# Kernel tuning notes

Hardware: AMD Instinct MI355X
Metric: run time of the kernel (lower is better)

Reference implementation:

```python
import jax, jax.numpy as jnp
import numpy as np

EPS = 1e-6
GROUPS = 32


def setup_inputs() -> dict:
    key = jax.random.key(0)
    ks = jax.random.split(key, 6)
    B, C, T = 4, 256, 4096
    s = 1.0 / np.sqrt(C)
    return {
        "x": jax.random.normal(ks[0], (B, C, T), dtype=jnp.float32),
        "gn_scale": jnp.ones((C,), jnp.float32),
        "gn_bias": jnp.zeros((C,), jnp.float32),
        "wq": jax.random.normal(ks[1], (C, C), jnp.float32) * s,
        "bq": jnp.zeros((C,), jnp.float32),
        "wk": jax.random.normal(ks[2], (C, C), jnp.float32) * s,
        "bk": jnp.zeros((C,), jnp.float32),
        "wv": jax.random.normal(ks[3], (C, C), jnp.float32) * s,
        "bv": jnp.zeros((C,), jnp.float32),
        "wo": jax.random.normal(ks[4], (C, C), jnp.float32) * s,
        "bo": jnp.zeros((C,), jnp.float32),
    }


def _group_norm(x, scale, bias):
    B, C, T = x.shape
    h = x.reshape(B, GROUPS, C // GROUPS, T)
    mean = h.mean(axis=(2, 3), keepdims=True)
    var = ((h - mean) ** 2).mean(axis=(2, 3), keepdims=True)
    h = (h - mean) * jax.lax.rsqrt(var + EPS)
    h = h.reshape(B, C, T)
    return h * scale[None, :, None] + bias[None, :, None]


def _conv1x1(w, b, h):
    # Conv1d kernel_size=1 == per-timestep channel matmul
    return jnp.einsum('oc,bct->bot', w, h) + b[None, :, None]


def reference(x, gn_scale, gn_bias, wq, bq, wk, bk, wv, bv, wo, bo):
    B, C, T = x.shape
    h = _group_norm(x, gn_scale, gn_bias)
    q = _conv1x1(wq, bq, h)  # [B,C,T]
    k = _conv1x1(wk, bk, h)
    v = _conv1x1(wv, bv, h)
    # w_[b,q,k] = sum_c q[b,c,q] k[b,c,k] * C**-0.5, softmax over k
    w = jnp.einsum('bcq,bck->bqk', q, k) * (C ** -0.5)
    w = jax.nn.softmax(w, axis=2)
    # torch code: h_[b, i, c] = sum_j w[b, j, i] * v_perm[b, j, c]
    h = jnp.einsum('bqk,bcq->bck', w, v)  # [B,C,T]
    h = _conv1x1(wo, bo, h)
    return x + h
```

## Files before the change

kernel.cpp:

```cpp
#include <hip/hip_runtime.h>

typedef float f32x4 __attribute__((ext_vector_type(4)));
typedef short s16x8 __attribute__((ext_vector_type(8)));

#define MOFF 12.0f

__device__ __forceinline__ unsigned short f2bf(float f) {
  unsigned int u = __float_as_uint(f);
  u += 0x7fffu + ((u >> 16) & 1u);
  return (unsigned short)(u >> 16);
}

template <typename T>
__device__ __forceinline__ void gload16(const T* g, T* l) {
  __builtin_amdgcn_global_load_lds(
      (const __attribute__((address_space(1))) void*)g,
      (__attribute__((address_space(3))) void*)l, 16, 0, 0);
}

__global__ __launch_bounds__(256) void gn_stats_k(const float* __restrict__ x,
                                                  float* __restrict__ meanv,
                                                  float* __restrict__ rstdv) {
  const int bg = blockIdx.x;
  const float4* base = (const float4*)(x + (size_t)bg * 8 * 4096);
  float s = 0.f, q = 0.f;
  for (int i = threadIdx.x; i < 8192; i += 256) {
    float4 v = base[i];
    s += v.x + v.y + v.z + v.w;
    q += v.x * v.x + v.y * v.y + v.z * v.z + v.w * v.w;
  }
  for (int o = 32; o; o >>= 1) { s += __shfl_down(s, o); q += __shfl_down(q, o); }
  __shared__ float ss[4], sq[4];
  const int wv = threadIdx.x >> 6;
  if ((threadIdx.x & 63) == 0) { ss[wv] = s; sq[wv] = q; }
  __syncthreads();
  if (threadIdx.x == 0) {
    s = ss[0] + ss[1] + ss[2] + ss[3];
    q = sq[0] + sq[1] + sq[2] + sq[3];
    float mu = s * (1.f / 32768.f);
    float var = q * (1.f / 32768.f) - mu * mu;
    meanv[bg] = mu;
    rstdv[bg] = rsqrtf(var + 1e-6f);
  }
}

__global__ __launch_bounds__(256) void gn_apply_t_k(const float* __restrict__ x,
    const float* __restrict__ gamma, const float* __restrict__ beta,
    const float* __restrict__ meanv, const float* __restrict__ rstdv,
    unsigned short* __restrict__ hT) {
  __shared__ unsigned short tile[64][72];
  const int b = blockIdx.z, c0 = blockIdx.y * 64, t0 = blockIdx.x * 64;
  const int tid = threadIdx.x;
  {
    const int tr = tid >> 4, tc = (tid & 15) * 4;
    const float* xb = x + ((size_t)b * 256 + c0) * 4096 + t0;
    for (int p2 = 0; p2 < 4; ++p2) {
      int cl = p2 * 16 + tr;
      int c = c0 + cl;
      int bg = b * 32 + (c >> 3);
      float ga = gamma[c] * rstdv[bg];
      float be = beta[c] - meanv[bg] * ga;
      float4 v = *(const float4*)(xb + (size_t)cl * 4096 + tc);
      tile[cl][tc + 0] = f2bf(v.x * ga + be);
      tile[cl][tc + 1] = f2bf(v.y * ga + be);
      tile[cl][tc + 2] = f2bf(v.z * ga + be);
      tile[cl][tc + 3] = f2bf(v.w * ga + be);
    }
  }
  __syncthreads();
  {
    const int orow = tid >> 3, oc = (tid & 7) * 8;
    unsigned short* hb = hT + ((size_t)b * 4096 + t0) * 256 + c0;
    for (int p2 = 0; p2 < 2; ++p2) {
      int tl = p2 * 32 + orow;
      s16x8 w;
#pragma unroll
      for (int j = 0; j < 8; ++j) w[j] = (short)tile[oc + j][tl];
      *(s16x8*)(hb + (size_t)tl * 256 + oc) = w;
    }
  }
}

enum { EPI_WT = 0, EPI_PB = 1, EPI_FIN = 3, EPI_PBR = 4 };

template <bool AF32, int EPI>
__global__ __launch_bounds__(256) void gemm64_k(
    const void* __restrict__ Ap, long long sA, int lda,
    const unsigned short* __restrict__ Bp, long long sB, int ldb,
    void* __restrict__ Op, long long sO, int ldo,
    const float* __restrict__ bias,
    const float* __restrict__ xadd, long long sX,
    float scale, int K) {
  __shared__ s16x8 lsA[4][64];
  __shared__ s16x8 lsB[4][64];
  const int tid = threadIdx.x;
  const int m0 = blockIdx.y * 64, n0 = blockIdx.x * 64;
  const int z = blockIdx.z;
  const int lane = tid & 63, wv = tid >> 6;
  const int lrow = lane & 15, lg = lane >> 4;
  const int srow = tid >> 2, scg = tid & 3;
  const int swrow = srow ^ (scg << 1);

  f32x4 acc[4];
#pragma unroll
  for (int i = 0; i < 4; ++i) acc[i] = (f32x4){0.f, 0.f, 0.f, 0.f};

  const unsigned short* Bb = Bp + (size_t)z * sB + (size_t)(n0 + srow) * ldb + scg * 8;

  for (int k0 = 0; k0 < K; k0 += 32) {
    if (AF32) {
      const float* ap = (const float*)Ap + (size_t)z * sA + (size_t)(m0 + srow) * lda + k0 + scg * 8;
      float4 v0 = *(const float4*)ap;
      float4 v1 = *(const float4*)(ap + 4);
      s16x8 w;
      w[0] = (short)f2bf(v0.x); w[1] = (short)f2bf(v0.y);
      w[2] = (short)f2bf(v0.z); w[3] = (short)f2bf(v0.w);
      w[4] = (short)f2bf(v1.x); w[5] = (short)f2bf(v1.y);
      w[6] = (short)f2bf(v1.z); w[7] = (short)f2bf(v1.w);
      lsA[scg][swrow] = w;
    } else {
      const unsigned short* ap = (const unsigned short*)Ap + (size_t)z * sA + (size_t)(m0 + srow) * lda + k0 + scg * 8;
      lsA[scg][swrow] = *(const s16x8*)ap;
    }
    lsB[scg][swrow] = *(const s16x8*)(Bb + k0);
    __syncthreads();
    s16x8 af = lsA[lg][(wv * 16 + lrow) ^ (lg << 1)];
#pragma unroll
    for (int nt = 0; nt < 4; ++nt) {
      s16x8 bf = lsB[lg][(nt * 16 + lrow) ^ (lg << 1)];
      acc[nt] = __builtin_amdgcn_mfma_f32_16x16x32_bf16(af, bf, acc[nt], 0, 0, 0);
    }
    __syncthreads();
  }

  const int mb = m0 + wv * 16 + lg * 4;
  float bv0 = 0.f, bv1 = 0.f, bv2 = 0.f, bv3 = 0.f;
  if (bias) { bv0 = bias[mb]; bv1 = bias[mb + 1]; bv2 = bias[mb + 2]; bv3 = bias[mb + 3]; }
#pragma unroll
  for (int nt = 0; nt < 4; ++nt) {
    const int n = n0 + nt * 16 + lrow;
    if (EPI == EPI_WT) {
      ushort4 pk;
      pk.x = f2bf((acc[nt][0] + bv0) * scale);
      pk.y = f2bf((acc[nt][1] + bv1) * scale);
      pk.z = f2bf((acc[nt][2] + bv2) * scale);
      pk.w = f2bf((acc[nt][3] + bv3) * scale);
      *(ushort4*)((unsigned short*)Op + (size_t)z * sO + (size_t)n * ldo + mb) = pk;
    } else if (EPI == EPI_PB) {
      unsigned short* o = (unsigned short*)Op + (size_t)z * sO;
      o[(size_t)(mb + 0) * ldo + n] = f2bf(acc[nt][0] + bv0);
      o[(size_t)(mb + 1) * ldo + n] = f2bf(acc[nt][1] + bv1);
      o[(size_t)(mb + 2) * ldo + n] = f2bf(acc[nt][2] + bv2);
      o[(size_t)(mb + 3) * ldo + n] = f2bf(acc[nt][3] + bv3);
    } else if (EPI == EPI_PBR) {
      unsigned short* o = (unsigned short*)Op + (size_t)z * sO;
      const float rc = (xadd + (size_t)z * sX)[n];
      o[(size_t)(mb + 0) * ldo + n] = f2bf((acc[nt][0] + bv0) * rc);
      o[(size_t)(mb + 1) * ldo + n] = f2bf((acc[nt][1] + bv1) * rc);
      o[(size_t)(mb + 2) * ldo + n] = f2bf((acc[nt][2] + bv2) * rc);
      o[(size_t)(mb + 3) * ldo + n] = f2bf((acc[nt][3] + bv3) * rc);
    } else {
      float* o = (float*)Op + (size_t)z * sO;
      const float* xa = xadd + (size_t)z * sX;
      o[(size_t)(mb + 0) * ldo + n] = acc[nt][0] + bv0 + xa[(size_t)(mb + 0) * ldo + n];
      o[(size_t)(mb + 1) * ldo + n] = acc[nt][1] + bv1 + xa[(size_t)(mb + 1) * ldo + n];
      o[(size_t)(mb + 2) * ldo + n] = acc[nt][2] + bv2 + xa[(size_t)(mb + 2) * ldo + n];
      o[(size_t)(mb + 3) * ldo + n] = acc[nt][3] + bv3 + xa[(size_t)(mb + 3) * ldo + n];
    }
  }
}

__global__ __launch_bounds__(256) void attn_stats3_k(
    const unsigned short* __restrict__ qT,
    const unsigned short* __restrict__ kT,
    float* __restrict__ pl) {
  __shared__ unsigned short kbuf[2][64 * 256];
  const int tid = threadIdx.x;
  const int b = blockIdx.z;
  const int Q0 = blockIdx.x * 256;
  const int kc = blockIdx.y;
  const int lane = tid & 63, wq = tid >> 6;
  const int lrow = lane & 15, lg = lane >> 4;

  const unsigned short* qb = qT + (size_t)b * (4096 * 256);
  const unsigned short* kb = kT + (size_t)b * (4096 * 256);

  s16x8 af[4][8];
#pragma unroll
  for (int mt = 0; mt < 4; ++mt)
#pragma unroll
    for (int ks = 0; ks < 8; ++ks)
      af[mt][ks] = *(const s16x8*)(qb + (size_t)(Q0 + wq * 64 + mt * 16 + lrow) * 256 + ks * 32 + lg * 8);

  float sl[4][4];
#pragma unroll
  for (int mt = 0; mt < 4; ++mt)
#pragma unroll
    for (int j = 0; j < 4; ++j) sl[mt][j] = 0.f;

  int cur = 0;
  {
    const unsigned short* src = kb + (size_t)(kc * 512) * 256;
#pragma unroll
    for (int rep = 0; rep < 8; ++rep) {
      int i = rep * 256 + tid;
      int row = i >> 5, c8 = i & 31;
      gload16(src + (size_t)row * 256 + (c8 ^ (row & 7)) * 8, &kbuf[0][(i - lane) * 8]);
    }
  }
  __syncthreads();

  for (int it = 0; it < 8; ++it) {
    if (it + 1 < 8) {
      const unsigned short* src = kb + (size_t)(kc * 512 + (it + 1) * 64) * 256;
#pragma unroll
      for (int rep = 0; rep < 8; ++rep) {
        int i = rep * 256 + tid;
        int row = i >> 5, c8 = i & 31;
        gload16(src + (size_t)row * 256 + (c8 ^ (row & 7)) * 8, &kbuf[cur ^ 1][(i - lane) * 8]);
      }
    }
#pragma unroll
    for (int nt = 0; nt < 4; ++nt) {
      f32x4 acc[4];
#pragma unroll
      for (int mt = 0; mt < 4; ++mt) acc[mt] = (f32x4){0.f, 0.f, 0.f, 0.f};
#pragma unroll
      for (int ks = 0; ks < 8; ++ks) {
        int row = nt * 16 + lrow;
        int ch = (ks * 4 + lg) ^ (row & 7);
        s16x8 bf = *(const s16x8*)&kbuf[cur][row * 256 + ch * 8];
#pragma unroll
        for (int mt = 0; mt < 4; ++mt)
          acc[mt] = __builtin_amdgcn_mfma_f32_16x16x32_bf16(af[mt][ks], bf, acc[mt], 0, 0, 0);
      }
#pragma unroll
      for (int mt = 0; mt < 4; ++mt)
#pragma unroll
        for (int j = 0; j < 4; ++j) sl[mt][j] += __expf(acc[mt][j] - MOFF);
    }
    __syncthreads();
    cur ^= 1;
  }
#pragma unroll
  for (int mt = 0; mt < 4; ++mt)
#pragma unroll
    for (int j = 0; j < 4; ++j) {
      float v = sl[mt][j];
      v += __shfl_xor(v, 1);
      v += __shfl_xor(v, 2);
      v += __shfl_xor(v, 4);
      v += __shfl_xor(v, 8);
      sl[mt][j] = v;
    }
  if (lrow == 0) {
    float* plb = pl + ((size_t)kc * 4 + b) * 4096;
#pragma unroll
    for (int mt = 0; mt < 4; ++mt)
#pragma unroll
      for (int j = 0; j < 4; ++j)
        plb[Q0 + wq * 64 + mt * 16 + lg * 4 + j] = sl[mt][j];
  }
}

__global__ __launch_bounds__(256) void make_r_k(const float* __restrict__ pl,
                                                float* __restrict__ ra) {
  int i = blockIdx.x * 256 + threadIdx.x;
  int b = i >> 12, q = i & 4095;
  float l = 0.f;
#pragma unroll
  for (int kc = 0; kc < 8; ++kc) l += pl[((size_t)kc * 4 + b) * 4096 + q];
  ra[i] = 1.f / l;
}

__global__ __launch_bounds__(512) void attn_pv6e_k(
    const unsigned short* __restrict__ qT,
    const unsigned short* __restrict__ kT,
    const unsigned short* __restrict__ vt,
    unsigned short* __restrict__ aT) {
  __shared__ unsigned short qbuf[2][64 * 256];
  __shared__ unsigned short P[64 * 64];
  const int tid = threadIdx.x;
  const int pidx = blockIdx.x;
  const int z = (pidx >> 1) & 3;
  const int kt = ((pidx >> 3) << 1) | (pidx & 1);
  const int K0 = kt * 64;
  const int lane = tid & 63, w = tid >> 6;
  const int lrow = lane & 15, lg = lane >> 4;
  const int khw = w >> 2;
  const int qqw = w & 3;

  const unsigned short* qg = qT + (size_t)z * (4096 * 256);
  const unsigned short* kg = kT + (size_t)z * (4096 * 256);
  const unsigned short* vg = vt + (size_t)z * (4096 * 256);

  s16x8 kf[2][8];
#pragma unroll
  for (int ktl = 0; ktl < 2; ++ktl)
#pragma unroll
    for (int ks = 0; ks < 8; ++ks)
      kf[ktl][ks] = *(const s16x8*)(kg + (size_t)(K0 + khw * 32 + ktl * 16 + lrow) * 256 + ks * 32 + lg * 8);

  f32x4 oacc[2][4];
#pragma unroll
  for (int ct = 0; ct < 2; ++ct)
#pragma unroll
    for (int nt = 0; nt < 4; ++nt) oacc[ct][nt] = (f32x4){0.f, 0.f, 0.f, 0.f};

  int cur = 0;
  {
#pragma unroll
    for (int rep = 0; rep < 4; ++rep) {
      int i = rep * 512 + tid;
      int row = i >> 5, c8 = i & 31;
      gload16(qg + (size_t)row * 256 + (c8 ^ (row & 7)) * 8, &qbuf[0][(i - lane) * 8]);
    }
  }
  __syncthreads();

  for (int qi = 0; qi < 64; ++qi) {
    const int q0 = qi * 64;
    s16x8 vf[2][2];
#pragma unroll
    for (int ct = 0; ct < 2; ++ct)
#pragma unroll
      for (int qs = 0; qs < 2; ++qs)
        vf[ct][qs] = *(const s16x8*)(vg + (size_t)(w * 32 + ct * 16 + lrow) * 4096 + q0 + qs * 32 + lg * 8);
    if (qi + 1 < 64) {
      const unsigned short* src = qg + (size_t)(q0 + 64) * 256;
#pragma unroll
      for (int rep = 0; rep < 4; ++rep) {
        int i = rep * 512 + tid;
        int row = i >> 5, c8 = i & 31;
        gload16(src + (size_t)row * 256 + (c8 ^ (row & 7)) * 8, &qbuf[cur ^ 1][(i - lane) * 8]);
      }
    }
    f32x4 sacc[2];
    sacc[0] = (f32x4){0.f, 0.f, 0.f, 0.f};
    sacc[1] = (f32x4){0.f, 0.f, 0.f, 0.f};
#pragma unroll
    for (int ks = 0; ks < 8; ++ks) {
      int row = qqw * 16 + lrow;
      int ch = (ks * 4 + lg) ^ (row & 7);
      s16x8 qf = *(const s16x8*)&qbuf[cur][row * 256 + ch * 8];
      sacc[0] = __builtin_amdgcn_mfma_f32_16x16x32_bf16(kf[0][ks], qf, sacc[0], 0, 0, 0);
      sacc[1] = __builtin_amdgcn_mfma_f32_16x16x32_bf16(kf[1][ks], qf, sacc[1], 0, 0, 0);
    }
    {
      const int ql = qqw * 16 + lrow;
#pragma unroll
      for (int ktl = 0; ktl < 2; ++ktl)
#pragma unroll
        for (int j = 0; j < 4; ++j) {
          int k = khw * 32 + ktl * 16 + lg * 4 + j;
          float p = __expf(sacc[ktl][j] - MOFF);
          P[k * 64 + (((ql >> 3) ^ (k & 7)) << 3) + (ql & 7)] = f2bf(p);
        }
    }
    __syncthreads();
#pragma unroll
    for (int qs = 0; qs < 2; ++qs) {
      s16x8 pf[4];
#pragma unroll
      for (int nt = 0; nt < 4; ++nt) {
        int k = nt * 16 + lrow;
        pf[nt] = *(const s16x8*)&P[k * 64 + (((qs * 4 + lg) ^ (k & 7)) << 3)];
      }
#pragma unroll
      for (int ct = 0; ct < 2; ++ct)
#pragma unroll
        for (int nt = 0; nt < 4; ++nt)
          oacc[ct][nt] = __builtin_amdgcn_mfma_f32_16x16x32_bf16(vf[ct][qs], pf[nt], oacc[ct][nt], 0, 0, 0);
    }
    __syncthreads();
    cur ^= 1;
  }
  unsigned short* ab = aT + (size_t)z * (4096 * 256);
#pragma unroll
  for (int ct = 0; ct < 2; ++ct)
#pragma unroll
    for (int nt = 0; nt < 4; ++nt) {
      int k = K0 + nt * 16 + lrow;
      int c = w * 32 + ct * 16 + lg * 4;
      ushort4 pk;
      pk.x = f2bf(oacc[ct][nt][0]);
      pk.y = f2bf(oacc[ct][nt][1]);
      pk.z = f2bf(oacc[ct][nt][2]);
      pk.w = f2bf(oacc[ct][nt][3]);
      *(ushort4*)(ab + (size_t)k * 256 + c) = pk;
    }
}

extern "C" void kernel_launch(void* const* d_in, const int* in_sizes, int n_in,
                              void* d_out, int out_size, void* d_ws, size_t ws_size,
                              hipStream_t stream) {
  const float* x   = (const float*)d_in[0];
  const float* gns = (const float*)d_in[1];
  const float* gnb = (const float*)d_in[2];
  const float* wq  = (const float*)d_in[3];
  const float* bq  = (const float*)d_in[4];
  const float* wk  = (const float*)d_in[5];
  const float* bk  = (const float*)d_in[6];
  const float* wvp = (const float*)d_in[7];
  const float* bv  = (const float*)d_in[8];
  const float* wo  = (const float*)d_in[9];
  const float* bo  = (const float*)d_in[10];
  float* out = (float*)d_out;

  const int B = 4, C = 256, T = 4096;
  const long long TCe = (long long)T * C;

  char* p = (char*)d_ws;
  unsigned short* hT = (unsigned short*)p; p += (size_t)B * TCe * 2;
  unsigned short* qT = (unsigned short*)p; p += (size_t)B * TCe * 2;
  unsigned short* kT = (unsigned short*)p; p += (size_t)B * TCe * 2;
  unsigned short* vb = (unsigned short*)p; p += (size_t)B * TCe * 2;
  unsigned short* aT = (unsigned short*)p; p += (size_t)B * TCe * 2;
  float* gmean = (float*)p; p += 512;
  float* grstd = (float*)p; p += 512;
  float* pl = (float*)p; p += (size_t)8 * B * T * 4;
  float* ra = (float*)p; p += (size_t)B * T * 4;

  gn_stats_k<<<B * 32, 256, 0, stream>>>(x, gmean, grstd);
  gn_apply_t_k<<<dim3(T / 64, C / 64, B), 256, 0, stream>>>(x, gns, gnb, gmean, grstd, hT);

  gemm64_k<true, EPI_WT><<<dim3(T / 64, C / 64, B), 256, 0, stream>>>(
      wq, 0, C, hT, TCe, C, qT, TCe, C, bq, nullptr, 0, 0.0625f, C);
  gemm64_k<true, EPI_WT><<<dim3(T / 64, C / 64, B), 256, 0, stream>>>(
      wk, 0, C, hT, TCe, C, kT, TCe, C, bk, nullptr, 0, 1.0f, C);

  attn_stats3_k<<<dim3(T / 256, 8, B), 256, 0, stream>>>(qT, kT, pl);
  make_r_k<<<B * T / 256, 256, 0, stream>>>(pl, ra);
  gemm64_k<true, EPI_PBR><<<dim3(T / 64, C / 64, B), 256, 0, stream>>>(
      wvp, 0, C, hT, TCe, C, vb, TCe, T, bv, ra, T, 1.0f, C);

  attn_pv6e_k<<<256, 512, 0, stream>>>(qT, kT, vb, aT);

  gemm64_k<true, EPI_FIN><<<dim3(T / 64, C / 64, B), 256, 0, stream>>>(
      wo, 0, C, aT, TCe, C, out, TCe, T, bo, x, TCe, 1.0f, C);
}
```

Baseline: 221.2 us.

## Split attention PV kernel over query halves with fp32 partials and merge kernel

The PV attention kernel is split along the query dimension into two halves, doubling the grid from 256 to 512 blocks so more work runs concurrently across CUs. Each half writes fp32 partial outputs to a new workspace buffer. A new merge kernel then sums the two halves and converts the result to bf16. This adds extra global memory traffic for the partials and one more kernel launch in exchange for better occupancy and a shorter per-block loop.

Result: slower. 234.2 us (+5.8%).

```diff
diff --git a/kernel.cpp b/kernel.cpp
--- a/kernel.cpp
+++ b/kernel.cpp
@@ -273,18 +273,21 @@
   ra[i] = 1.f / l;
 }
 
-__global__ __launch_bounds__(512) void attn_pv6e_k(
+__global__ __launch_bounds__(512) void attn_pv6g_k(
     const unsigned short* __restrict__ qT,
     const unsigned short* __restrict__ kT,
     const unsigned short* __restrict__ vt,
-    unsigned short* __restrict__ aT) {
+    float* __restrict__ po) {
   __shared__ unsigned short qbuf[2][64 * 256];
   __shared__ unsigned short P[64 * 64];
   const int tid = threadIdx.x;
   const int pidx = blockIdx.x;
-  const int z = (pidx >> 1) & 3;
-  const int kt = ((pidx >> 3) << 1) | (pidx & 1);
+  const int qh = pidx >> 8;
+  const int rest = pidx & 255;
+  const int z = (rest >> 1) & 3;
+  const int kt = ((rest >> 3) << 1) | (rest & 1);
   const int K0 = kt * 64;
+  const int QB = qh * 2048;
   const int lane = tid & 63, w = tid >> 6;
   const int lrow = lane & 15, lg = lane >> 4;
   const int khw = w >> 2;
@@ -313,20 +316,20 @@
     for (int rep = 0; rep < 4; ++rep) {
       int i = rep * 512 + tid;
       int row = i >> 5, c8 = i & 31;
-      gload16(qg + (size_t)row * 256 + (c8 ^ (row & 7)) * 8, &qbuf[0][(i - lane) * 8]);
+      gload16(qg + (size_t)(QB + row) * 256 + (c8 ^ (row & 7)) * 8, &qbuf[0][(i - lane) * 8]);
     }
   }
   __syncthreads();
 
-  for (int qi = 0; qi < 64; ++qi) {
-    const int q0 = qi * 64;
+  for (int qi = 0; qi < 32; ++qi) {
+    const int q0 = QB + qi * 64;
     s16x8 vf[2][2];
 #pragma unroll
     for (int ct = 0; ct < 2; ++ct)
 #pragma unroll
       for (int qs = 0; qs < 2; ++qs)
         vf[ct][qs] = *(const s16x8*)(vg + (size_t)(w * 32 + ct * 16 + lrow) * 4096 + q0 + qs * 32 + lg * 8);
-    if (qi + 1 < 64) {
+    if (qi + 1 < 32) {
       const unsigned short* src = qg + (size_t)(q0 + 64) * 256;
 #pragma unroll
       for (int rep = 0; rep < 4; ++rep) {
@@ -375,20 +378,35 @@
     __syncthreads();
     cur ^= 1;
   }
-  unsigned short* ab = aT + (size_t)z * (4096 * 256);
+  float* ob = po + (((size_t)(z * 2 + qh)) * 4096) * 256;
 #pragma unroll
   for (int ct = 0; ct < 2; ++ct)
 #pragma unroll
     for (int nt = 0; nt < 4; ++nt) {
       int k = K0 + nt * 16 + lrow;
       int c = w * 32 + ct * 16 + lg * 4;
-      ushort4 pk;
-      pk.x = f2bf(oacc[ct][nt][0]);
-      pk.y = f2bf(oacc[ct][nt][1]);
-      pk.z = f2bf(oacc[ct][nt][2]);
-      pk.w = f2bf(oacc[ct][nt][3]);
-      *(ushort4*)(ab + (size_t)k * 256 + c) = pk;
-    }
+      *(float4*)(ob + (size_t)k * 256 + c) = (float4){oacc[ct][nt][0], oacc[ct][nt][1],
+                                                      oacc[ct][nt][2], oacc[ct][nt][3]};
+    }
+}
+
+__global__ __launch_bounds__(256) void merge2_k(const float* __restrict__ po,
+                                                unsigned short* __restrict__ aT) {
+  const size_t i = (size_t)blockIdx.x * 256 + threadIdx.x;
+  const size_t n4 = (size_t)4096 * 64;
+  const int b = (int)(i / n4);
+  const size_t r = i - (size_t)b * n4;
+  const float4* p = (const float4*)(po + ((size_t)b * 2) * 4096 * 256) + r;
+  const size_t st = (size_t)4096 * 64;
+  float4 s0 = p[0], s1 = p[st];
+  float4 s;
+  s.x = s0.x + s1.x;
+  s.y = s0.y + s1.y;
+  s.z = s0.z + s1.z;
+  s.w = s0.w + s1.w;
+  ushort4 o;
+  o.x = f2bf(s.x); o.y = f2bf(s.y); o.z = f2bf(s.z); o.w = f2bf(s.w);
+  *(ushort4*)(aT + (size_t)b * 4096 * 256 + r * 4) = o;
 }
 
 extern "C" void kernel_launch(void* const* d_in, const int* in_sizes, int n_in,
@@ -420,6 +438,7 @@
   float* grstd = (float*)p; p += 512;
   float* pl = (float*)p; p += (size_t)8 * B * T * 4;
   float* ra = (float*)p; p += (size_t)B * T * 4;
+  float* po = (float*)p; p += (size_t)B * 2 * TCe * 4;
 
   gn_stats_k<<<B * 32, 256, 0, stream>>>(x, gmean, grstd);
   gn_apply_t_k<<<dim3(T / 64, C / 64, B), 256, 0, stream>>>(x, gns, gnb, gmean, grstd, hT);
@@ -434,7 +453,8 @@
   gemm64_k<true, EPI_PBR><<<dim3(T / 64, C / 64, B), 256, 0, stream>>>(
       wvp, 0, C, hT, TCe, C, vb, TCe, T, bv, ra, T, 1.0f, C);
 
-  attn_pv6e_k<<<256, 512, 0, stream>>>(qT, kT, vb, aT);
+  attn_pv6g_k<<<512, 512, 0, stream>>>(qT, kT, vb, po);
+  merge2_k<<<(int)((size_t)B * TCe / 4 / 256), 256, 0, stream>>>(po, aT);
 
   gemm64_k<true, EPI_FIN><<<dim3(T / 64, C / 64, B), 256, 0, stream>>>(
       wo, 0, C, aT, TCe, C, out, TCe, T, bo, x, TCe, 1.0f, C);
```
